# Kernel optimization log

Hardware: AMD Instinct MI355X
Metric: run time of the kernel (lower is better)

## Reference

```python
import jax, jax.numpy as jnp
import numpy as np

N, E = 50000, 800000
D_IN, H, D_OUT = 64, 64, 32
NEG_SLOPE = 0.2


def setup_inputs() -> dict:
    key = jax.random.key(0)
    ks = jax.random.split(key, 20)
    inp = {
        "x": jax.random.normal(ks[0], (N, D_IN), dtype=jnp.float32),
        "edge_index": jax.random.randint(ks[1], (2, E), 0, N, dtype=jnp.int32),
    }
    def lin(k, fan_in, fan_out):
        s = 1.0 / np.sqrt(fan_in)
        return jax.random.uniform(k, (fan_in, fan_out), jnp.float32, -s, s)
    # GAT layer params: W [in,H], att_src [H], att_dst [H], bias [H]
    dims_in = [D_IN, H, H]
    for i in range(3):
        inp[f"W{i+1}"] = lin(ks[2 + 4 * i], dims_in[i], H)
        inp[f"a_src{i+1}"] = jax.random.normal(ks[3 + 4 * i], (H,), jnp.float32) * 0.1
        inp[f"a_dst{i+1}"] = jax.random.normal(ks[4 + 4 * i], (H,), jnp.float32) * 0.1
        inp[f"b{i+1}"] = jnp.zeros((H,), jnp.float32)
    inp["lin1_W"] = lin(ks[14], H, H)
    inp["lin1_b"] = jnp.zeros((H,), jnp.float32)
    inp["lin2_W"] = lin(ks[15], H, D_OUT)
    inp["lin2_b"] = jnp.zeros((D_OUT,), jnp.float32)
    return inp


def gat_layer(x, src, dst, W, a_src, a_dst, b):
    h = x @ W                                   # [N, H]
    alpha_s = (h * a_src).sum(-1)               # [N]
    alpha_d = (h * a_dst).sum(-1)               # [N]
    e = jax.nn.leaky_relu(alpha_s[src] + alpha_d[dst], NEG_SLOPE)  # [E]
    m = jax.lax.stop_gradient(jax.ops.segment_max(e, dst, num_segments=N))
    w = jnp.exp(e - m[dst])                     # [E]
    denom = jax.ops.segment_sum(w, dst, num_segments=N)
    alpha = w / denom[dst]                      # segment softmax over incoming edges
    out = jax.ops.segment_sum(alpha[:, None] * h[src], dst, num_segments=N)
    return out + b


def reference(x, edge_index, W1, a_src1, a_dst1, b1, W2, a_src2, a_dst2, b2,
              W3, a_src3, a_dst3, b3, lin1_W, lin1_b, lin2_W, lin2_b):
    src, dst = edge_index[0], edge_index[1]
    h = jax.nn.relu(gat_layer(x, src, dst, W1, a_src1, a_dst1, b1))
    h = jax.nn.relu(gat_layer(h, src, dst, W2, a_src2, a_dst2, b2))
    h = jax.nn.relu(gat_layer(h, src, dst, W3, a_src3, a_dst3, b3))
    h = jax.nn.relu(h @ lin1_W + lin1_b)
    return h @ lin2_W + lin2_b
```

## Files before the change

kernel.cpp:

```cpp
#include <hip/hip_runtime.h>

#define NEG_SLOPE 0.2f
#define NBUCK 256

template <bool RELU, bool WANT_ALPHA>
__global__ __launch_bounds__(256) void gemm64(
    const float* __restrict__ x, const float* __restrict__ W,
    const float* __restrict__ bias,
    const float* __restrict__ a_src, const float* __restrict__ a_dst,
    float* __restrict__ out, float* __restrict__ alpha_s,
    float* __restrict__ alpha_d, int N)
{
    __shared__ float Xs[64][68];
    __shared__ float Ws[64][64];

    const int row0 = blockIdx.x * 64;

    for (int i = threadIdx.x; i < 1024; i += 256)
        ((float4*)Ws)[i] = ((const float4*)W)[i];
    for (int i = threadIdx.x; i < 1024; i += 256) {
        int r = i >> 4, c4 = (i & 15) * 4;
        float4 v = {0.f, 0.f, 0.f, 0.f};
        if (row0 + r < N) v = *(const float4*)&x[(size_t)(row0 + r) * 64 + c4];
        *(float4*)&Xs[r][c4] = v;
    }
    __syncthreads();

    const int tx = threadIdx.x & 15;
    const int ty = threadIdx.x >> 4;

    float acc[4][4] = {{0.f,0.f,0.f,0.f},{0.f,0.f,0.f,0.f},
                       {0.f,0.f,0.f,0.f},{0.f,0.f,0.f,0.f}};

#pragma unroll 8
    for (int k = 0; k < 64; ++k) {
        const float4 wv = *(const float4*)&Ws[k][tx * 4];
        const float x0 = Xs[ty * 4 + 0][k];
        const float x1 = Xs[ty * 4 + 1][k];
        const float x2 = Xs[ty * 4 + 2][k];
        const float x3 = Xs[ty * 4 + 3][k];
        acc[0][0] += x0 * wv.x; acc[0][1] += x0 * wv.y;
        acc[0][2] += x0 * wv.z; acc[0][3] += x0 * wv.w;
        acc[1][0] += x1 * wv.x; acc[1][1] += x1 * wv.y;
        acc[1][2] += x1 * wv.z; acc[1][3] += x1 * wv.w;
        acc[2][0] += x2 * wv.x; acc[2][1] += x2 * wv.y;
        acc[2][2] += x2 * wv.z; acc[2][3] += x2 * wv.w;
        acc[3][0] += x3 * wv.x; acc[3][1] += x3 * wv.y;
        acc[3][2] += x3 * wv.z; acc[3][3] += x3 * wv.w;
    }

    float4 bv = {0.f, 0.f, 0.f, 0.f};
    if (bias) bv = *(const float4*)&bias[tx * 4];

#pragma unroll
    for (int i = 0; i < 4; ++i) {
        const int r = row0 + ty * 4 + i;
        if (r < N) {
            float4 o;
            o.x = acc[i][0] + bv.x; o.y = acc[i][1] + bv.y;
            o.z = acc[i][2] + bv.z; o.w = acc[i][3] + bv.w;
            if (RELU) {
                o.x = fmaxf(o.x, 0.f); o.y = fmaxf(o.y, 0.f);
                o.z = fmaxf(o.z, 0.f); o.w = fmaxf(o.w, 0.f);
            }
            *(float4*)&out[(size_t)r * 64 + tx * 4] = o;
        }
    }

    if (WANT_ALPHA) {
        const float4 asv = *(const float4*)&a_src[tx * 4];
        const float4 adv = *(const float4*)&a_dst[tx * 4];
#pragma unroll
        for (int i = 0; i < 4; ++i) {
            float s = acc[i][0]*asv.x + acc[i][1]*asv.y
                    + acc[i][2]*asv.z + acc[i][3]*asv.w;
            float d = acc[i][0]*adv.x + acc[i][1]*adv.y
                    + acc[i][2]*adv.z + acc[i][3]*adv.w;
#pragma unroll
            for (int off = 1; off < 16; off <<= 1) {
                s += __shfl_xor(s, off, 16);
                d += __shfl_xor(d, off, 16);
            }
            const int r = row0 + ty * 4 + i;
            if (tx == 0 && r < N) { alpha_s[r] = s; alpha_d[r] = d; }
        }
    }
}

__global__ __launch_bounds__(256) void gemm_head(
    const float* __restrict__ X, const float* __restrict__ W1,
    const float* __restrict__ b1, const float* __restrict__ W2,
    const float* __restrict__ b2, float* __restrict__ out, int N)
{
    __shared__ float Xs[64][68];
    __shared__ float W1s[64][64];
    __shared__ float W2s[64][32];

    const int row0 = blockIdx.x * 64;

    for (int i = threadIdx.x; i < 1024; i += 256)
        ((float4*)W1s)[i] = ((const float4*)W1)[i];
    for (int i = threadIdx.x; i < 512; i += 256)
        ((float4*)W2s)[i] = ((const float4*)W2)[i];
    for (int i = threadIdx.x; i < 1024; i += 256) {
        int r = i >> 4, c4 = (i & 15) * 4;
        float4 v = {0.f, 0.f, 0.f, 0.f};
        if (row0 + r < N) v = *(const float4*)&X[(size_t)(row0 + r) * 64 + c4];
        *(float4*)&Xs[r][c4] = v;
    }
    __syncthreads();

    const int tx = threadIdx.x & 15;
    const int ty = threadIdx.x >> 4;

    float acc[4][4] = {{0.f,0.f,0.f,0.f},{0.f,0.f,0.f,0.f},
                       {0.f,0.f,0.f,0.f},{0.f,0.f,0.f,0.f}};
#pragma unroll 8
    for (int k = 0; k < 64; ++k) {
        const float4 wv = *(const float4*)&W1s[k][tx * 4];
        const float x0 = Xs[ty * 4 + 0][k];
        const float x1 = Xs[ty * 4 + 1][k];
        const float x2 = Xs[ty * 4 + 2][k];
        const float x3 = Xs[ty * 4 + 3][k];
        acc[0][0] += x0 * wv.x; acc[0][1] += x0 * wv.y;
        acc[0][2] += x0 * wv.z; acc[0][3] += x0 * wv.w;
        acc[1][0] += x1 * wv.x; acc[1][1] += x1 * wv.y;
        acc[1][2] += x1 * wv.z; acc[1][3] += x1 * wv.w;
        acc[2][0] += x2 * wv.x; acc[2][1] += x2 * wv.y;
        acc[2][2] += x2 * wv.z; acc[2][3] += x2 * wv.w;
        acc[3][0] += x3 * wv.x; acc[3][1] += x3 * wv.y;
        acc[3][2] += x3 * wv.z; acc[3][3] += x3 * wv.w;
    }

    const float4 bv = *(const float4*)&b1[tx * 4];
    __syncthreads();
#pragma unroll
    for (int i = 0; i < 4; ++i) {
        Xs[ty * 4 + i][tx * 4 + 0] = fmaxf(acc[i][0] + bv.x, 0.f);
        Xs[ty * 4 + i][tx * 4 + 1] = fmaxf(acc[i][1] + bv.y, 0.f);
        Xs[ty * 4 + i][tx * 4 + 2] = fmaxf(acc[i][2] + bv.z, 0.f);
        Xs[ty * 4 + i][tx * 4 + 3] = fmaxf(acc[i][3] + bv.w, 0.f);
    }
    __syncthreads();

    float a2[4][2] = {{0.f,0.f},{0.f,0.f},{0.f,0.f},{0.f,0.f}};
#pragma unroll 8
    for (int k = 0; k < 64; ++k) {
        const float2 wv = *(const float2*)&W2s[k][tx * 2];
        const float t0 = Xs[ty * 4 + 0][k];
        const float t1 = Xs[ty * 4 + 1][k];
        const float t2 = Xs[ty * 4 + 2][k];
        const float t3 = Xs[ty * 4 + 3][k];
        a2[0][0] += t0 * wv.x; a2[0][1] += t0 * wv.y;
        a2[1][0] += t1 * wv.x; a2[1][1] += t1 * wv.y;
        a2[2][0] += t2 * wv.x; a2[2][1] += t2 * wv.y;
        a2[3][0] += t3 * wv.x; a2[3][1] += t3 * wv.y;
    }
    const float2 b2v = *(const float2*)&b2[tx * 2];
#pragma unroll
    for (int i = 0; i < 4; ++i) {
        const int r = row0 + ty * 4 + i;
        if (r < N) {
            float2 o;
            o.x = a2[i][0] + b2v.x;
            o.y = a2[i][1] + b2v.y;
            *(float2*)&out[(size_t)r * 32 + tx * 2] = o;
        }
    }
}

__global__ __launch_bounds__(256) void bucket_hist(
    const int* __restrict__ ei, int E, int* __restrict__ bhist)
{
    __shared__ int h[NBUCK];
    const int t = threadIdx.x;
    h[t] = 0;
    __syncthreads();
    for (int e = blockIdx.x * 256 + t; e < E; e += gridDim.x * 256)
        atomicAdd(&h[((unsigned)ei[E + e]) >> 8], 1);
    __syncthreads();
    if (h[t]) atomicAdd(&bhist[t], h[t]);
}

#define PC_EPT 8
#define PC_TILE 2048
__global__ __launch_bounds__(256) void partition_coarse(
    const int* __restrict__ ei, int E, const int* __restrict__ bhist,
    int* __restrict__ gcurs, int* __restrict__ pairs)
{
    __shared__ int sc[NBUCK];
    __shared__ int hist[NBUCK];
    __shared__ int base[NBUCK];
    const int t = threadIdx.x;

    const int bh = bhist[t];
    sc[t] = bh; __syncthreads();
    for (int off = 1; off < 256; off <<= 1) {
        int v = sc[t];
        if (t >= off) v += sc[t - off];
        __syncthreads(); sc[t] = v; __syncthreads();
    }
    const int bbase = sc[t] - bh;
    hist[t] = 0;
    __syncthreads();

    const int tile0 = blockIdx.x * PC_TILE;
    int sv[PC_EPT], dv[PC_EPT], rk[PC_EPT];
#pragma unroll
    for (int i = 0; i < PC_EPT; ++i) {
        const int e = tile0 + i * 256 + t;
        if (e < E) {
            sv[i] = ei[e];
            dv[i] = ei[E + e];
            rk[i] = atomicAdd(&hist[dv[i] >> 8], 1);
        } else dv[i] = -1;
    }
    __syncthreads();
    if (hist[t] > 0) base[t] = bbase + atomicAdd(&gcurs[t], hist[t]);
    __syncthreads();
#pragma unroll
    for (int i = 0; i < PC_EPT; ++i) {
        if (dv[i] >= 0) {
            const int b = dv[i] >> 8;
            pairs[base[b] + rk[i]] = sv[i] | ((dv[i] & 255) << 16);
        }
    }
}

__global__ __launch_bounds__(256) void fine_scatter(
    const int* __restrict__ bhist, const int* __restrict__ pairs,
    int N, int E, int* __restrict__ row_off, int* __restrict__ csr_src)
{
    __shared__ int sc[NBUCK];
    __shared__ int cnt[NBUCK];
    __shared__ int cur[NBUCK];
    const int t = threadIdx.x, b = blockIdx.x;

    const int bh = bhist[t];
    sc[t] = bh; __syncthreads();
    for (int off = 1; off < 256; off <<= 1) {
        int v = sc[t];
        if (t >= off) v += sc[t - off];
        __syncthreads(); sc[t] = v; __syncthreads();
    }
    sc[t] -= bh;
    cnt[t] = 0;
    __syncthreads();

    const int sb = sc[b];
    const int se = sb + bhist[b];

    for (int p = sb + t; p < se; p += 256)
        atomicAdd(&cnt[pairs[p] >> 16], 1);
    __syncthreads();

    const int c = cnt[t];
    cur[t] = c; __syncthreads();
    for (int off = 1; off < 256; off <<= 1) {
        int v = cur[t];
        if (t >= off) v += cur[t - off];
        __syncthreads(); cur[t] = v; __syncthreads();
    }
    const int node_off = sb + cur[t] - c;
    __syncthreads();
    cur[t] = node_off;
    const int n = b * 256 + t;
    if (n < N) row_off[n] = node_off;
    if (b == gridDim.x - 1 && t == 0) row_off[N] = E;
    __syncthreads();

    for (int p = sb + t; p < se; p += 256) {
        const int v = pairs[p];
        const int pos = atomicAdd(&cur[v >> 16], 1);
        csr_src[pos] = v & 0xFFFF;
    }
}

__global__ __launch_bounds__(256) void gat_aggregate(
    const int* __restrict__ row_off, const int* __restrict__ csr_src,
    const float* __restrict__ h, const float* __restrict__ as,
    const float* __restrict__ ad, const float* __restrict__ bias,
    float* __restrict__ out, int N)
{
    const int wv = (blockIdx.x * 256 + threadIdx.x) >> 6;
    if (wv >= N) return;
    const int d    = wv;
    const int lane = threadIdx.x & 63;
    const int g    = lane >> 4;
    const int gl   = lane & 15;

    const int beg = row_off[d], end = row_off[d + 1];
    const float add = ad[d];

    float  den = 0.f;
    float4 acc = {0.f, 0.f, 0.f, 0.f};

    int srcp = (beg + g < end) ? csr_src[beg + g] : 0;

    for (int e0 = beg; e0 < end; e0 += 4) {
        const bool valid = (e0 + g < end);
        const int  s     = srcp;
        const int  en    = e0 + 4 + g;
        srcp = (en < end) ? csr_src[en] : 0;

        const float av = as[s];
        const float4 hv = *(const float4*)&h[(size_t)s * 64 + gl * 4];

        float ev = av + add;
        ev = (ev >= 0.f) ? ev : NEG_SLOPE * ev;
        const float w = valid ? __expf(ev) : 0.f;

        den += w;
        acc.x += w * hv.x; acc.y += w * hv.y;
        acc.z += w * hv.z; acc.w += w * hv.w;
    }

#pragma unroll
    for (int off = 16; off <= 32; off <<= 1) {
        acc.x += __shfl_xor(acc.x, off, 64);
        acc.y += __shfl_xor(acc.y, off, 64);
        acc.z += __shfl_xor(acc.z, off, 64);
        acc.w += __shfl_xor(acc.w, off, 64);
        den   += __shfl_xor(den,   off, 64);
    }

    if (g == 0) {
        const float4 bvv = *(const float4*)&bias[gl * 4];
        const float inv = (den > 0.f) ? (1.f / den) : 0.f;
        float4 o;
        o.x = fmaxf(acc.x * inv + bvv.x, 0.f);
        o.y = fmaxf(acc.y * inv + bvv.y, 0.f);
        o.z = fmaxf(acc.z * inv + bvv.z, 0.f);
        o.w = fmaxf(acc.w * inv + bvv.w, 0.f);
        *(float4*)&out[(size_t)d * 64 + gl * 4] = o;
    }
}

extern "C" void kernel_launch(void* const* d_in, const int* in_sizes, int n_in,
                              void* d_out, int out_size, void* d_ws, size_t ws_size,
                              hipStream_t stream)
{
    const float* x  = (const float*)d_in[0];
    const int*   ei = (const int*)d_in[1];
    const float* W[3]    = {(const float*)d_in[2], (const float*)d_in[6],  (const float*)d_in[10]};
    const float* asrc[3] = {(const float*)d_in[3], (const float*)d_in[7],  (const float*)d_in[11]};
    const float* adst[3] = {(const float*)d_in[4], (const float*)d_in[8],  (const float*)d_in[12]};
    const float* bia[3]  = {(const float*)d_in[5], (const float*)d_in[9],  (const float*)d_in[13]};
    const float* lin1W = (const float*)d_in[14];
    const float* lin1b = (const float*)d_in[15];
    const float* lin2W = (const float*)d_in[16];
    const float* lin2b = (const float*)d_in[17];

    const int N = in_sizes[0] / 64;
    const int E = in_sizes[1] / 2;
    const int B = (N + 255) / 256;

    float* X       = (float*)d_ws;
    float* H       = X + (size_t)N * 64;
    float* AS      = H + (size_t)N * 64;
    float* AD      = AS + N;
    int*   row_off = (int*)(AD + N);
    int*   csr_src = row_off + (N + 1);
    int*   bhist   = csr_src + E;
    int*   gcurs   = bhist + 256;
    int*   pairs   = (int*)H;

    const int g64_grid = (N + 63) / 64;
    const int agg_grid = (N + 3) / 4;
    const int pc_grid  = (E + PC_TILE - 1) / PC_TILE;

    hipMemsetAsync(bhist, 0, 512 * sizeof(int), stream);
    bucket_hist<<<256, 256, 0, stream>>>(ei, E, bhist);
    partition_coarse<<<pc_grid, 256, 0, stream>>>(ei, E, bhist, gcurs, pairs);
    fine_scatter<<<B, 256, 0, stream>>>(bhist, pairs, N, E, row_off, csr_src);

    for (int l = 0; l < 3; ++l) {
        const float* in_act = (l == 0) ? x : X;
        gemm64<false, true><<<g64_grid, 256, 0, stream>>>(
            in_act, W[l], nullptr, asrc[l], adst[l], H, AS, AD, N);
        gat_aggregate<<<agg_grid, 256, 0, stream>>>(
            row_off, csr_src, H, AS, AD, bia[l], X, N);
    }

    gemm_head<<<g64_grid, 256, 0, stream>>>(
        X, lin1W, lin1b, lin2W, lin2b, (float*)d_out, N);
}
```

Baseline: 227.1 us.

## Fuse edge histogram into first GEMM and slice aggregation by feature columns

The standalone bucket histogram kernel is removed. Its work now runs in the first 256 blocks of the layer-1 GEMM, which saves a launch and overlaps it with the matmul. The edge pairs buffer moves out of H into its own workspace region so layer 1's H output is not overwritten. Aggregation is split into four column slices of 16 features, each wave handling 16 edges at a time with 4 lanes per edge. This is meant to raise parallelism and let slices share L2 for gathers, but it recomputes the softmax weights four times and quadruples the csr/alpha loads.

```diff
diff --git a/kernel.cpp b/kernel.cpp
--- a/kernel.cpp
+++ b/kernel.cpp
@@ -3,16 +3,17 @@
 #define NEG_SLOPE 0.2f
 #define NBUCK 256
 
-template <bool RELU, bool WANT_ALPHA>
+template <bool WANT_ALPHA, bool DO_HIST>
 __global__ __launch_bounds__(256) void gemm64(
     const float* __restrict__ x, const float* __restrict__ W,
-    const float* __restrict__ bias,
     const float* __restrict__ a_src, const float* __restrict__ a_dst,
     float* __restrict__ out, float* __restrict__ alpha_s,
-    float* __restrict__ alpha_d, int N)
+    float* __restrict__ alpha_d, int N,
+    const int* __restrict__ ei, int E, int* __restrict__ bhist)
 {
     __shared__ float Xs[64][68];
     __shared__ float Ws[64][64];
+    __shared__ int   hsh[NBUCK];
 
     const int row0 = blockIdx.x * 64;
 
@@ -24,6 +25,7 @@
         if (row0 + r < N) v = *(const float4*)&x[(size_t)(row0 + r) * 64 + c4];
         *(float4*)&Xs[r][c4] = v;
     }
+    if (DO_HIST && blockIdx.x < 256) hsh[threadIdx.x] = 0;
     __syncthreads();
 
     const int tx = threadIdx.x & 15;
@@ -49,20 +51,11 @@
         acc[3][2] += x3 * wv.z; acc[3][3] += x3 * wv.w;
     }
 
-    float4 bv = {0.f, 0.f, 0.f, 0.f};
-    if (bias) bv = *(const float4*)&bias[tx * 4];
-
 #pragma unroll
     for (int i = 0; i < 4; ++i) {
         const int r = row0 + ty * 4 + i;
         if (r < N) {
-            float4 o;
-            o.x = acc[i][0] + bv.x; o.y = acc[i][1] + bv.y;
-            o.z = acc[i][2] + bv.z; o.w = acc[i][3] + bv.w;
-            if (RELU) {
-                o.x = fmaxf(o.x, 0.f); o.y = fmaxf(o.y, 0.f);
-                o.z = fmaxf(o.z, 0.f); o.w = fmaxf(o.w, 0.f);
-            }
+            float4 o = {acc[i][0], acc[i][1], acc[i][2], acc[i][3]};
             *(float4*)&out[(size_t)r * 64 + tx * 4] = o;
         }
     }
@@ -84,6 +77,14 @@
             const int r = row0 + ty * 4 + i;
             if (tx == 0 && r < N) { alpha_s[r] = s; alpha_d[r] = d; }
         }
+    }
+
+    if (DO_HIST && blockIdx.x < 256) {
+        __syncthreads();
+        for (int e = blockIdx.x * 256 + threadIdx.x; e < E; e += 256 * 256)
+            atomicAdd(&hsh[((unsigned)ei[E + e]) >> 8], 1);
+        __syncthreads();
+        if (hsh[threadIdx.x]) atomicAdd(&bhist[threadIdx.x], hsh[threadIdx.x]);
     }
 }
 
@@ -113,8 +114,7 @@
     const int tx = threadIdx.x & 15;
     const int ty = threadIdx.x >> 4;
 
-    float acc[4][4] = {{0.f,0.f,0.f,0.f},{0.f,0.f,0.f,0.f},
-                       {0.f,0.f,0.f,0.f},{0.f,0.f,0.f,0.f}};
+    float acc[4][4] = {{0,0,0,0},{0,0,0,0},{0,0,0,0},{0,0,0,0}};
 #pragma unroll 8
     for (int k = 0; k < 64; ++k) {
         const float4 wv = *(const float4*)&W1s[k][tx * 4];
@@ -143,7 +143,7 @@
     }
     __syncthreads();
 
-    float a2[4][2] = {{0.f,0.f},{0.f,0.f},{0.f,0.f},{0.f,0.f}};
+    float a2[4][2] = {{0,0},{0,0},{0,0},{0,0}};
 #pragma unroll 8
     for (int k = 0; k < 64; ++k) {
         const float2 wv = *(const float2*)&W2s[k][tx * 2];
@@ -169,19 +169,6 @@
     }
 }
 
-__global__ __launch_bounds__(256) void bucket_hist(
-    const int* __restrict__ ei, int E, int* __restrict__ bhist)
-{
-    __shared__ int h[NBUCK];
-    const int t = threadIdx.x;
-    h[t] = 0;
-    __syncthreads();
-    for (int e = blockIdx.x * 256 + t; e < E; e += gridDim.x * 256)
-        atomicAdd(&h[((unsigned)ei[E + e]) >> 8], 1);
-    __syncthreads();
-    if (h[t]) atomicAdd(&bhist[t], h[t]);
-}
-
 #define PC_EPT 8
 #define PC_TILE 2048
 __global__ __launch_bounds__(256) void partition_coarse(
@@ -276,18 +263,21 @@
     }
 }
 
-__global__ __launch_bounds__(256) void gat_aggregate(
+__global__ __launch_bounds__(256) void gat_aggregate_sliced(
     const int* __restrict__ row_off, const int* __restrict__ csr_src,
     const float* __restrict__ h, const float* __restrict__ as,
     const float* __restrict__ ad, const float* __restrict__ bias,
-    float* __restrict__ out, int N)
-{
-    const int wv = (blockIdx.x * 256 + threadIdx.x) >> 6;
-    if (wv >= N) return;
-    const int d    = wv;
+    float* __restrict__ out, int N, int nchunks)
+{
+    const int slice = blockIdx.x / nchunks;
+    const int chunk = blockIdx.x % nchunks;
+    const int d     = chunk * 4 + (threadIdx.x >> 6);
+    if (d >= N) return;
+
     const int lane = threadIdx.x & 63;
-    const int g    = lane >> 4;
-    const int gl   = lane & 15;
+    const int g    = lane >> 2;
+    const int gl   = lane & 3;
+    const int col0 = slice * 16 + gl * 4;
 
     const int beg = row_off[d], end = row_off[d + 1];
     const float add = ad[d];
@@ -295,16 +285,15 @@
     float  den = 0.f;
     float4 acc = {0.f, 0.f, 0.f, 0.f};
 
-    int srcp = (beg + g < end) ? csr_src[beg + g] : 0;
-
-    for (int e0 = beg; e0 < end; e0 += 4) {
+    int sp = (beg + g < end) ? csr_src[beg + g] : 0;
+
+    for (int e0 = beg; e0 < end; e0 += 16) {
         const bool valid = (e0 + g < end);
-        const int  s     = srcp;
-        const int  en    = e0 + 4 + g;
-        srcp = (en < end) ? csr_src[en] : 0;
-
-        const float av = as[s];
-        const float4 hv = *(const float4*)&h[(size_t)s * 64 + gl * 4];
+        const int  s     = sp;
+        sp = (e0 + 16 + g < end) ? csr_src[e0 + 16 + g] : 0;
+
+        const float  av = as[s];
+        const float4 hv = *(const float4*)&h[(size_t)s * 64 + col0];
 
         float ev = av + add;
         ev = (ev >= 0.f) ? ev : NEG_SLOPE * ev;
@@ -316,7 +305,7 @@
     }
 
 #pragma unroll
-    for (int off = 16; off <= 32; off <<= 1) {
+    for (int off = 4; off <= 32; off <<= 1) {
         acc.x += __shfl_xor(acc.x, off, 64);
         acc.y += __shfl_xor(acc.y, off, 64);
         acc.z += __shfl_xor(acc.z, off, 64);
@@ -325,14 +314,14 @@
     }
 
     if (g == 0) {
-        const float4 bvv = *(const float4*)&bias[gl * 4];
+        const float4 bvv = *(const float4*)&bias[col0];
         const float inv = (den > 0.f) ? (1.f / den) : 0.f;
         float4 o;
         o.x = fmaxf(acc.x * inv + bvv.x, 0.f);
         o.y = fmaxf(acc.y * inv + bvv.y, 0.f);
         o.z = fmaxf(acc.z * inv + bvv.z, 0.f);
         o.w = fmaxf(acc.w * inv + bvv.w, 0.f);
-        *(float4*)&out[(size_t)d * 64 + gl * 4] = o;
+        *(float4*)&out[(size_t)d * 64 + col0] = o;
     }
 }
 
@@ -363,23 +352,29 @@
     int*   csr_src = row_off + (N + 1);
     int*   bhist   = csr_src + E;
     int*   gcurs   = bhist + 256;
-    int*   pairs   = (int*)H;
+    int*   pairs   = gcurs + 256;
 
     const int g64_grid = (N + 63) / 64;
-    const int agg_grid = (N + 3) / 4;
+    const int nchunks  = (N + 3) / 4;
+    const int agg_grid = 4 * nchunks;
     const int pc_grid  = (E + PC_TILE - 1) / PC_TILE;
 
     hipMemsetAsync(bhist, 0, 512 * sizeof(int), stream);
-    bucket_hist<<<256, 256, 0, stream>>>(ei, E, bhist);
+
+    gemm64<true, true><<<g64_grid, 256, 0, stream>>>(
+        x, W[0], asrc[0], adst[0], H, AS, AD, N, ei, E, bhist);
+
     partition_coarse<<<pc_grid, 256, 0, stream>>>(ei, E, bhist, gcurs, pairs);
     fine_scatter<<<B, 256, 0, stream>>>(bhist, pairs, N, E, row_off, csr_src);
 
-    for (int l = 0; l < 3; ++l) {
-        const float* in_act = (l == 0) ? x : X;
-        gemm64<false, true><<<g64_grid, 256, 0, stream>>>(
-            in_act, W[l], nullptr, asrc[l], adst[l], H, AS, AD, N);
-        gat_aggregate<<<agg_grid, 256, 0, stream>>>(
-            row_off, csr_src, H, AS, AD, bia[l], X, N);
+    gat_aggregate_sliced<<<agg_grid, 256, 0, stream>>>(
+        row_off, csr_src, H, AS, AD, bia[0], X, N, nchunks);
+
+    for (int l = 1; l < 3; ++l) {
+        gemm64<true, false><<<g64_grid, 256, 0, stream>>>(
+            X, W[l], asrc[l], adst[l], H, AS, AD, N, nullptr, 0, nullptr);
+        gat_aggregate_sliced<<<agg_grid, 256, 0, stream>>>(
+            row_off, csr_src, H, AS, AD, bia[l], X, N, nchunks);
     }
 
     gemm_head<<<g64_grid, 256, 0, stream>>>(
```

After: 314.2 us. 38.4% more time.
